# Optimization experiments

Hardware: AMD Instinct MI355X
Metric: run time of the kernel (lower is better)

## Reference

```python
import jax, jax.numpy as jnp
import numpy as np

DIM = 512
HEADS = 8
DHEAD = DIM // 8          # 64
INNER = HEADS * DHEAD     # 512
M_LANDMARKS = 256
PINV_ITERS = 6
KSZ = 33                  # residual depthwise conv kernel (default)


def setup_inputs() -> dict:
    key = jax.random.key(0)
    ks = jax.random.split(key, 5)
    B, N = 1, 16384
    s = DIM ** -0.5
    return {
        "x": jax.random.normal(ks[0], (B, N, DIM), jnp.float32),
        "norm_w": jnp.ones((DIM,), jnp.float32),
        "norm_b": jnp.zeros((DIM,), jnp.float32),
        "w_qkv": jax.random.normal(ks[1], (3 * INNER, DIM), jnp.float32) * s,   # Linear(dim, 3*inner, bias=False)
        "w_out": jax.random.normal(ks[2], (DIM, INNER), jnp.float32) * s,        # Linear(inner, dim)
        "b_out": jnp.zeros((DIM,), jnp.float32),
        "conv_w": jax.random.normal(ks[3], (HEADS, 1, KSZ, 1), jnp.float32) * 0.1,  # depthwise Conv2d(h,h,(33,1),groups=h)
    }


def _layernorm(x, w, b, eps=1e-5):
    mu = x.mean(-1, keepdims=True)
    var = ((x - mu) ** 2).mean(-1, keepdims=True)
    return (x - mu) * jax.lax.rsqrt(var + eps) * w + b


def _moore_penrose_pinv(a, iters):
    # a: [B, H, m, m]; matches lucidrains moore_penrose_iter_pinv (global max over col/row sums)
    abs_a = jnp.abs(a)
    col = abs_a.sum(-1).max()
    row = abs_a.sum(-2).max()
    z = jnp.swapaxes(a, -1, -2) / (col * row)
    I = jnp.eye(a.shape[-1], dtype=a.dtype)
    for _ in range(iters):
        az = a @ z
        z = 0.25 * z @ (13 * I - az @ (15 * I - az @ (7 * I - az)))
    return z


def _nystrom_attention(h, w_qkv, w_out, b_out, conv_w):
    B, N, _ = h.shape
    qkv = h @ w_qkv.T                          # [B, N, 3*inner]
    q, k, v = jnp.split(qkv, 3, axis=-1)

    def heads(t):
        return t.reshape(B, N, HEADS, DHEAD).transpose(0, 2, 1, 3)  # [B, H, N, d]
    q = heads(q) * (DHEAD ** -0.5)
    k = heads(k)
    v = heads(v)

    # landmark pooling: mean over contiguous groups of size l = N / m
    l = N // M_LANDMARKS
    q_l = q.reshape(B, HEADS, M_LANDMARKS, l, DHEAD).mean(3)   # [B, H, m, d]
    k_l = k.reshape(B, HEADS, M_LANDMARKS, l, DHEAD).mean(3)

    attn1 = jax.nn.softmax(jnp.einsum('bhnd,bhmd->bhnm', q, k_l), axis=-1)      # [B,H,N,m]
    attn2 = jax.nn.softmax(jnp.einsum('bhid,bhjd->bhij', q_l, k_l), axis=-1)    # [B,H,m,m]
    attn3 = jax.nn.softmax(jnp.einsum('bhmd,bhnd->bhmn', q_l, k), axis=-1)      # [B,H,m,N]

    attn2_inv = _moore_penrose_pinv(attn2, PINV_ITERS)
    out = attn1 @ (attn2_inv @ (attn3 @ v))                                     # [B,H,N,d]

    # residual depthwise conv along sequence dim (kernel 33x1, groups=HEADS, no bias)
    conv = jax.lax.conv_general_dilated(
        v, conv_w, window_strides=(1, 1),
        padding=((KSZ // 2, KSZ // 2), (0, 0)),
        dimension_numbers=('NCHW', 'OIHW', 'NCHW'),
        feature_group_count=HEADS)
    out = out + conv

    out = out.transpose(0, 2, 1, 3).reshape(B, N, INNER)
    return out @ w_out.T + b_out


def reference(x, norm_w, norm_b, w_qkv, w_out, b_out, conv_w):
    h = _layernorm(x, norm_w, norm_b)
    return x + _nystrom_attention(h, w_qkv, w_out, b_out, conv_w)
```

## Files before the change

### kernel.cpp

```cpp
#include <hip/hip_runtime.h>
#include <hip/hip_bf16.h>


typedef __attribute__((ext_vector_type(8))) short bf16x8;
typedef __attribute__((ext_vector_type(4))) float f32x4;

#define MFMA16(A, B, C) __builtin_amdgcn_mfma_f32_16x16x32_bf16(A, B, C, 0, 0, 0)
#define GLD16(g, l) __builtin_amdgcn_global_load_lds( \
    (const __attribute__((address_space(1))) void*)(g), \
    (__attribute__((address_space(3))) void*)(l), 16, 0, 0)

static __device__ __forceinline__ unsigned short f2b(float f) {
  __hip_bfloat16 h = __float2bfloat16(f);
  return *reinterpret_cast<unsigned short*>(&h);
}
static __device__ __forceinline__ float b2f(unsigned short u) {
  return __uint_as_float(((unsigned)u) << 16);
}

__global__ __launch_bounds__(256) void k_init(const float* __restrict__ x,
    const float* __restrict__ nw, const float* __restrict__ nb,
    unsigned short* __restrict__ h,
    const float* __restrict__ wq, unsigned short* __restrict__ wqb,
    const float* __restrict__ wo, unsigned short* __restrict__ wob) {
  const int b = blockIdx.x;
  const int t = threadIdx.x;
  if (b < 8192) {
    const int row = b * 2 + (t >> 7);
    const int tl = t & 127;
    const float4 xv = ((const float4*)(x + (size_t)row * 512))[tl];
    float s  = xv.x + xv.y + xv.z + xv.w;
    float sq = xv.x*xv.x + xv.y*xv.y + xv.z*xv.z + xv.w*xv.w;
    #pragma unroll
    for (int o = 32; o > 0; o >>= 1) {
      s  += __shfl_down(s, o, 64);
      sq += __shfl_down(sq, o, 64);
    }
    __shared__ float ls[4], lq[4];
    if ((t & 63) == 0) { ls[t >> 6] = s; lq[t >> 6] = sq; }
    __syncthreads();
    const int base = (t >> 7) << 1;
    s = ls[base] + ls[base + 1]; sq = lq[base] + lq[base + 1];
    const float mean = s * (1.0f / 512.0f);
    const float var  = sq * (1.0f / 512.0f) - mean * mean;
    const float rstd = rsqrtf(var + 1e-5f);
    const float4 wv = ((const float4*)nw)[tl];
    const float4 bv = ((const float4*)nb)[tl];
    ushort4 hv;
    hv.x = f2b((xv.x - mean) * rstd * wv.x + bv.x);
    hv.y = f2b((xv.y - mean) * rstd * wv.y + bv.y);
    hv.z = f2b((xv.z - mean) * rstd * wv.z + bv.z);
    hv.w = f2b((xv.w - mean) * rstd * wv.w + bv.w);
    ((ushort4*)(h + (size_t)row * 512))[tl] = hv;
  } else if (b < 8960) {
    const int i = (b - 8192) * 256 + t;
    const float4 f = ((const float4*)wq)[i];
    ushort4 u;
    u.x = f2b(f.x); u.y = f2b(f.y); u.z = f2b(f.z); u.w = f2b(f.w);
    ((ushort4*)wqb)[i] = u;
  } else {
    const int i = (b - 8960) * 256 + t;
    const float4 f = ((const float4*)wo)[i];
    ushort4 u;
    u.x = f2b(f.x); u.y = f2b(f.y); u.z = f2b(f.z); u.w = f2b(f.w);
    ((ushort4*)wob)[i] = u;
  }
}

__global__ __launch_bounds__(256) void k_qkv_mfma(const unsigned short* __restrict__ A,
    const unsigned short* __restrict__ B,
    unsigned short* __restrict__ qb, unsigned short* __restrict__ kb,
    unsigned short* __restrict__ vb) {
  __shared__ __align__(16) unsigned short SB[8192];
  unsigned short* As = SB;
  unsigned short* Bs = SB + 4096;
  const int t = threadIdx.x;
  const int lane = t & 63, w = t >> 6;
  const int quad = lane >> 4, l15 = lane & 15;
  const int wm = (w >> 1) * 64, wn = (w & 1) * 64;
  const int bid = blockIdx.x;
  const int xcd = bid & 7, i0 = bid >> 3;
  const int by = xcd * 16 + i0 / 12, bx = i0 % 12;
  const int m0 = by * 128, n0 = bx * 128;
  f32x4 acc[4][4];
  #pragma unroll
  for (int i = 0; i < 4; ++i)
    #pragma unroll
    for (int j = 0; j < 4; ++j) acc[i][j] = (f32x4){0.f, 0.f, 0.f, 0.f};
  for (int k0 = 0; k0 < 512; k0 += 32) {
    __syncthreads();
    #pragma unroll
    for (int c = 0; c < 2; ++c) {
      const int slot = c * 256 + t;
      const int row = slot >> 2, seg = slot & 3;
      GLD16(A + (size_t)(m0 + row) * 512 + k0 + seg * 8, As + slot * 8);
      GLD16(B + (size_t)(n0 + row) * 512 + k0 + seg * 8, Bs + slot * 8);
    }
    __syncthreads();
    bf16x8 a[4], b[4];
    #pragma unroll
    for (int i = 0; i < 4; ++i)
      a[i] = *(const bf16x8*)(As + (wm + i * 16 + l15) * 32 + quad * 8);
    #pragma unroll
    for (int j = 0; j < 4; ++j)
      b[j] = *(const bf16x8*)(Bs + (wn + j * 16 + l15) * 32 + quad * 8);
    #pragma unroll
    for (int i = 0; i < 4; ++i)
      #pragma unroll
      for (int j = 0; j < 4; ++j)
        acc[i][j] = MFMA16(a[i], b[j], acc[i][j]);
  }
  #pragma unroll
  for (int hf = 0; hf < 2; ++hf) {
    const int colbase = n0 + hf * 64;
    const int part = colbase >> 9;
    const int head = (colbase & 511) >> 6;
    unsigned short* dst = (part == 0) ? qb : (part == 1) ? kb : vb;
    const float scale = (part == 0) ? 0.125f : 1.0f;
    __syncthreads();
    if ((w & 1) == hf) {
      #pragma unroll
      for (int i = 0; i < 4; ++i)
        #pragma unroll
        for (int j = 0; j < 4; ++j)
          #pragma unroll
          for (int r = 0; r < 4; ++r) {
            const int row = wm + i * 16 + quad * 4 + r;
            const int col = j * 16 + l15;
            SB[row * 64 + col] = f2b(acc[i][j][r] * scale);
          }
    }
    __syncthreads();
    const int row = t >> 1, seg = (t & 1) * 32;
    unsigned short* dp = dst + ((size_t)head * 16384 + m0 + row) * 64 + seg;
    #pragma unroll
    for (int kk = 0; kk < 4; ++kk)
      *(ulonglong2*)(dp + kk * 8) = *(const ulonglong2*)&SB[row * 64 + seg + kk * 8];
  }
}

__global__ __launch_bounds__(256) void k_prep(const unsigned short* __restrict__ vb,
    unsigned short* __restrict__ vt, const unsigned short* __restrict__ qb,
    const unsigned short* __restrict__ kb, float* __restrict__ qlf,
    unsigned short* __restrict__ qlb, float* __restrict__ klf,
    unsigned short* __restrict__ klb) {
  __shared__ __align__(16) unsigned char smem[64 * 72 * 2];
  const int t = threadIdx.x;
  const int h = blockIdx.y;
  if (blockIdx.z == 0) {
    auto T = (unsigned short(*)[72])smem;
    const int n0 = blockIdx.x * 64;
    const int n = t >> 2, sg = (t & 3) * 16;
    const unsigned short* p = vb + ((size_t)(h * 16384 + n0 + n)) * 64 + sg;
    #pragma unroll
    for (int i = 0; i < 16; i += 4) {
      const ushort4 u = *(const ushort4*)(p + i);
      T[sg + i + 0][n] = u.x; T[sg + i + 1][n] = u.y;
      T[sg + i + 2][n] = u.z; T[sg + i + 3][n] = u.w;
    }
    __syncthreads();
    const int d = t >> 2, so = (t & 3) * 16;
    unsigned short* q = vt + ((size_t)(h * 64 + d)) * 16384 + n0 + so;
    #pragma unroll
    for (int i = 0; i < 16; i += 4) {
      ushort4 u;
      u.x = T[d][so + i]; u.y = T[d][so + i + 1];
      u.z = T[d][so + i + 2]; u.w = T[d][so + i + 3];
      *(ushort4*)(q + i) = u;
    }
  } else {
    auto red = (float(*)[64])smem;
    const int d = t & 63, grp = t >> 6;
    const int m = blockIdx.x;
    const unsigned short* src = (blockIdx.z == 1) ? qb : kb;
    const unsigned short* p = src + ((size_t)h * 16384 + m * 64 + grp * 16) * 64 + d;
    float s = 0.f;
    #pragma unroll
    for (int i = 0; i < 16; ++i) s += b2f(p[(size_t)i * 64]);
    red[grp][d] = s;
    __syncthreads();
    if (t < 64) {
      float v = (red[0][d] + red[1][d]) + (red[2][d] + red[3][d]);
      v *= (1.0f / 64.0f);
      const size_t oi = ((size_t)h * 256 + m) * 64 + d;
      if (blockIdx.z == 1) { qlf[oi] = v; qlb[oi] = f2b(v); }
      else                 { klf[oi] = v; klb[oi] = f2b(v); }
    }
  }
}

__global__ __launch_bounds__(256) void k_attn2(const float* __restrict__ ql,
    const float* __restrict__ kl, float* __restrict__ a2, unsigned short* __restrict__ a2b,
    float* __restrict__ csum) {
  const int i = blockIdx.x, h = blockIdx.y, j = threadIdx.x;
  __shared__ float qrow[64];
  __shared__ float wred[4];
  __shared__ float wsum[4];
  if (j < 64) qrow[j] = ql[((size_t)h * 256 + i) * 64 + j];
  __syncthreads();
  const float* kr = kl + ((size_t)h * 256 + j) * 64;
  float s = 0.f;
  #pragma unroll 8
  for (int d = 0; d < 64; ++d) s += qrow[d] * kr[d];
  float mx = s;
  #pragma unroll
  for (int o2 = 32; o2 > 0; o2 >>= 1) mx = fmaxf(mx, __shfl_xor(mx, o2, 64));
  if ((j & 63) == 0) wred[j >> 6] = mx;
  __syncthreads();
  mx = fmaxf(fmaxf(wred[0], wred[1]), fmaxf(wred[2], wred[3]));
  const float e = __expf(s - mx);
  float sm = e;
  #pragma unroll
  for (int o2 = 32; o2 > 0; o2 >>= 1) sm += __shfl_xor(sm, o2, 64);
  if ((j & 63) == 0) wsum[j >> 6] = sm;
  __syncthreads();
  sm = wsum[0] + wsum[1] + wsum[2] + wsum[3];
  const float v = e / sm;
  const size_t idx = ((size_t)h * 256 + i) * 256 + j;
  a2[idx] = v;
  a2b[idx] = f2b(v);
  atomicAdd(&csum[h * 256 + j], v);
}

__global__ __launch_bounds__(256) void k_z0(const float* __restrict__ a2,
    const float* __restrict__ csum, unsigned short* __restrict__ z0b,
    unsigned short* __restrict__ z0t) {
  __shared__ float T[64][65];
  __shared__ float wm[4];
  const int bi = blockIdx.x, bj = blockIdx.y, h = blockIdx.z;
  const int t = threadIdx.x;
  const int r = t >> 2, cseg = (t & 3) * 16;
  float m = 0.f;
  #pragma unroll
  for (int c = 0; c < 8; ++c) m = fmaxf(m, csum[c * 256 + t]);
  #pragma unroll
  for (int o2 = 32; o2 > 0; o2 >>= 1) m = fmaxf(m, __shfl_xor(m, o2, 64));
  if ((t & 63) == 0) wm[t >> 6] = m;
  __syncthreads();
  const float g = fmaxf(fmaxf(wm[0], wm[1]), fmaxf(wm[2], wm[3]));
  const float inv = 1.0f / g;
  const float* p = a2 + ((size_t)h * 256 + bj * 64 + r) * 256 + bi * 64 + cseg;
  unsigned short* qt = z0t + ((size_t)h * 256 + bj * 64 + r) * 256 + bi * 64 + cseg;
  #pragma unroll
  for (int i = 0; i < 16; i += 4) {
    const float4 f = *(const float4*)(p + i);
    T[cseg + i + 0][r] = f.x; T[cseg + i + 1][r] = f.y;
    T[cseg + i + 2][r] = f.z; T[cseg + i + 3][r] = f.w;
    ushort4 u;
    u.x = f2b(f.x * inv); u.y = f2b(f.y * inv);
    u.z = f2b(f.z * inv); u.w = f2b(f.w * inv);
    *(ushort4*)(qt + i) = u;
  }
  __syncthreads();
  unsigned short* qb_ = z0b + ((size_t)h * 256 + bi * 64 + r) * 256 + bj * 64 + cseg;
  #pragma unroll
  for (int i = 0; i < 16; i += 4) {
    ushort4 u;
    u.x = f2b(T[r][cseg + i] * inv);     u.y = f2b(T[r][cseg + i + 1] * inv);
    u.z = f2b(T[r][cseg + i + 2] * inv); u.w = f2b(T[r][cseg + i + 3] * inv);
    *(ushort4*)(qb_ + i) = u;
  }
}

__global__ __launch_bounds__(256) void k_pgemm(const unsigned short* __restrict__ A,
    const unsigned short* __restrict__ Bt, unsigned short* __restrict__ Cn,
    unsigned short* __restrict__ Ct, float* __restrict__ Cf,
    float alpha, float sdiag, int use_diag) {
  __shared__ unsigned short As[64 * 256];
  __shared__ unsigned short Bs[32 * 256];
  const int t = threadIdx.x;
  const int lane = t & 63, w = t >> 6;
  const int quad = lane >> 4, l15 = lane & 15;
  const int bn = blockIdx.x, bm = blockIdx.y, h = blockIdx.z;
  const size_t hs = (size_t)h * 65536;
  const unsigned short* Ap = A + hs + (size_t)(bm * 64) * 256;
  const unsigned short* Bp = Bt + hs + (size_t)(bn * 32) * 256;
  #pragma unroll
  for (int c = 0; c < 8; ++c) {
    const int s = c * 256 + t;
    const int row = s >> 5, pc = s & 31;
    const int lc = pc ^ (row & 7);
    GLD16(Ap + (size_t)row * 256 + lc * 8, As + s * 8);
  }
  #pragma unroll
  for (int c = 0; c < 4; ++c) {
    const int s = c * 256 + t;
    const int row = s >> 5, pc = s & 31;
    const int lc = pc ^ (row & 7);
    GLD16(Bp + (size_t)row * 256 + lc * 8, Bs + s * 8);
  }
  f32x4 acc[2];
  acc[0] = (f32x4){0.f, 0.f, 0.f, 0.f};
  acc[1] = (f32x4){0.f, 0.f, 0.f, 0.f};
  __syncthreads();
  const int arow = w * 16 + l15;
  #pragma unroll
  for (int kc = 0; kc < 8; ++kc) {
    const bf16x8 a = *(const bf16x8*)(As + arow * 256 + (((kc * 4 + quad) ^ (arow & 7)) * 8));
    #pragma unroll
    for (int j = 0; j < 2; ++j) {
      const int brow = j * 16 + l15;
      const bf16x8 b = *(const bf16x8*)(Bs + brow * 256 + (((kc * 4 + quad) ^ (brow & 7)) * 8));
      acc[j] = MFMA16(a, b, acc[j]);
    }
  }
  const int row0 = bm * 64 + w * 16 + quad * 4;
  #pragma unroll
  for (int j = 0; j < 2; ++j) {
    const int col = bn * 32 + j * 16 + l15;
    float v[4];
    #pragma unroll
    for (int r = 0; r < 4; ++r) v[r] = acc[j][r] * alpha;
    if (Cn) {
      #pragma unroll
      for (int r = 0; r < 4; ++r) Cn[hs + (size_t)(row0 + r) * 256 + col] = f2b(v[r]);
    }
    if (Cf) {
      #pragma unroll
      for (int r = 0; r < 4; ++r) Cf[hs + (size_t)(row0 + r) * 256 + col] = v[r];
    }
    ushort4 u;
    float tv[4];
    #pragma unroll
    for (int r = 0; r < 4; ++r)
      tv[r] = use_diag ? ((col == row0 + r ? sdiag : 0.f) - v[r]) : v[r];
    u.x = f2b(tv[0]); u.y = f2b(tv[1]); u.z = f2b(tv[2]); u.w = f2b(tv[3]);
    *(ushort4*)(Ct + hs + (size_t)col * 256 + row0) = u;
  }
}

__global__ __launch_bounds__(256) void k_gemm256(const float* __restrict__ A,
    const float* __restrict__ B, float* __restrict__ C,
    float alpha, float sdiag, int use_diag) {
  A += (size_t)blockIdx.z * 65536;
  B += (size_t)blockIdx.z * 65536;
  C += (size_t)blockIdx.z * 65536;
  __shared__ float As[16][68];
  __shared__ float Bs[16][36];
  const int t = threadIdx.x, tx = t & 15, ty = t >> 4;
  const int bn = blockIdx.x, bm = blockIdx.y;
  const int lr = t >> 2, lk = (t & 3) << 2;
  const int bkr = t >> 4, bnc = (t & 15) << 1;
  float acc[4][2] = {{0.f}};
  for (int k0 = 0; k0 < 256; k0 += 16) {
    float4 a4 = *(const float4*)(A + (size_t)(bm * 64 + lr) * 256 + k0 + lk);
    float2 b2 = *(const float2*)(B + (size_t)(k0 + bkr) * 256 + bn * 32 + bnc);
    if (use_diag) {
      const int kg = k0 + bkr, ngb = bn * 32 + bnc;
      b2.x = (kg == ngb + 0 ? sdiag : 0.f) - b2.x;
      b2.y = (kg == ngb + 1 ? sdiag : 0.f) - b2.y;
    }
    __syncthreads();
    As[lk+0][lr] = a4.x; As[lk+1][lr] = a4.y; As[lk+2][lr] = a4.z; As[lk+3][lr] = a4.w;
    Bs[bkr][bnc] = b2.x; Bs[bkr][bnc + 1] = b2.y;
    __syncthreads();
    #pragma unroll
    for (int kq = 0; kq < 16; ++kq) {
      const float4 av = *(const float4*)&As[kq][ty << 2];
      const float bx_ = Bs[kq][tx << 1], by_ = Bs[kq][(tx << 1) + 1];
      acc[0][0] += av.x * bx_; acc[0][1] += av.x * by_;
      acc[1][0] += av.y * bx_; acc[1][1] += av.y * by_;
      acc[2][0] += av.z * bx_; acc[2][1] += av.z * by_;
      acc[3][0] += av.w * bx_; acc[3][1] += av.w * by_;
    }
  }
  #pragma unroll
  for (int ii = 0; ii < 4; ++ii)
    #pragma unroll
    for (int jj = 0; jj < 2; ++jj)
      C[(size_t)(bm * 64 + (ty << 2) + ii) * 256 + bn * 32 + (tx << 1) + jj] =
          alpha * acc[ii][jj];
}

__global__ __launch_bounds__(256) void k_gemmD(const float* __restrict__ A,
    const float* __restrict__ B, const float* __restrict__ rs,
    unsigned short* __restrict__ dtb) {
  __shared__ float Asf[16 * 68];
  __shared__ float Bsf[16 * 68];
  const int bm = blockIdx.x, h = blockIdx.y;
  A += (size_t)h * 65536;
  B += (size_t)h * 16384;
  rs += (size_t)h * 256;
  const int t = threadIdx.x, tx = t & 15, ty = t >> 4;
  const int lr = t >> 2, lk = (t & 3) << 2;
  const int bkr = t >> 4, bnc = (t & 15) << 2;
  float acc[4][4] = {{0.f}};
  for (int k0 = 0; k0 < 256; k0 += 16) {
    float4 a4 = *(const float4*)(A + (size_t)(bm * 64 + lr) * 256 + k0 + lk);
    float4 b4 = *(const float4*)(B + (size_t)(k0 + bkr) * 64 + bnc);
    const float rv = 1.0f / rs[k0 + bkr];
    b4.x *= rv; b4.y *= rv; b4.z *= rv; b4.w *= rv;
    __syncthreads();
    Asf[(lk + 0) * 68 + lr] = a4.x; Asf[(lk + 1) * 68 + lr] = a4.y;
    Asf[(lk + 2) * 68 + lr] = a4.z; Asf[(lk + 3) * 68 + lr] = a4.w;
    *(float4*)&Bsf[bkr * 68 + bnc] = b4;
    __syncthreads();
    #pragma unroll
    for (int kq = 0; kq < 16; ++kq) {
      const float4 av = *(const float4*)&Asf[kq * 68 + (ty << 2)];
      const float4 bv = *(const float4*)&Bsf[kq * 68 + (tx << 2)];
      acc[0][0] += av.x*bv.x; acc[0][1] += av.x*bv.y; acc[0][2] += av.x*bv.z; acc[0][3] += av.x*bv.w;
      acc[1][0] += av.y*bv.x; acc[1][1] += av.y*bv.y; acc[1][2] += av.y*bv.z; acc[1][3] += av.y*bv.w;
      acc[2][0] += av.z*bv.x; acc[2][1] += av.z*bv.y; acc[2][2] += av.z*bv.z; acc[2][3] += av.z*bv.w;
      acc[3][0] += av.w*bv.x; acc[3][1] += av.w*bv.y; acc[3][2] += av.w*bv.z; acc[3][3] += av.w*bv.w;
    }
  }
  #pragma unroll
  for (int ii = 0; ii < 4; ++ii)
    #pragma unroll
    for (int jj = 0; jj < 4; ++jj)
      dtb[(size_t)(h * 64 + (tx << 2) + jj) * 256 + bm * 64 + (ty << 2) + ii] =
          f2b(acc[ii][jj]);
}

__global__ __launch_bounds__(256) void k_w3_mfma(const unsigned short* __restrict__ qlb,
    const unsigned short* __restrict__ kb, const unsigned short* __restrict__ vt,
    float* __restrict__ W, float* __restrict__ lsum) {
  __shared__ unsigned short QLs[64 * 64];
  __shared__ unsigned short Ks [64 * 64];
  __shared__ unsigned short Vts[64 * 64];
  __shared__ unsigned short Ps [64 * 64];
  const int t = threadIdx.x;
  const int lane = t & 63, w = t >> 6;
  const int quad = lane >> 4, l15 = lane & 15;
  const int kc = blockIdx.x, mt = blockIdx.y, h = blockIdx.z;
  #pragma unroll
  for (int c = 0; c < 2; ++c) {
    const int slot = c * 256 + t;
    const int row = slot >> 3, pc = slot & 7, lc = pc ^ (row & 7);
    GLD16(qlb + ((size_t)(h * 256 + mt * 64 + row)) * 64 + lc * 8, QLs + slot * 8);
  }
  __syncthreads();
  const int arow = w * 16 + l15;
  const bf16x8 aq0 = *(const bf16x8*)(QLs + arow * 64 + ((quad    ) ^ (arow & 7)) * 8);
  const bf16x8 aq1 = *(const bf16x8*)(QLs + arow * 64 + ((quad + 4) ^ (arow & 7)) * 8);
  f32x4 wacc[4];
  #pragma unroll
  for (int dt = 0; dt < 4; ++dt) wacc[dt] = (f32x4){0.f, 0.f, 0.f, 0.f};
  float lacc[4] = {0.f, 0.f, 0.f, 0.f};
  for (int ss = 0; ss < 16; ++ss) {
    const int n0 = kc * 1024 + ss * 64;
    __syncthreads();
    #pragma unroll
    for (int c = 0; c < 2; ++c) {
      const int slot = c * 256 + t;
      const int row = slot >> 3, pc = slot & 7, lc = pc ^ (row & 7);
      GLD16(kb + ((size_t)(h * 16384 + n0 + row)) * 64 + lc * 8, Ks + slot * 8);
      GLD16(vt + ((size_t)(h * 64 + row)) * 16384 + n0 + lc * 8, Vts + slot * 8);
    }
    __syncthreads();
    f32x4 s[4];
    #pragma unroll
    for (int j = 0; j < 4; ++j) {
      s[j] = (f32x4){0.f, 0.f, 0.f, 0.f};
      const int brow = j * 16 + l15;
      const bf16x8 b0 = *(const bf16x8*)(Ks + brow * 64 + ((quad    ) ^ (brow & 7)) * 8);
      const bf16x8 b1 = *(const bf16x8*)(Ks + brow * 64 + ((quad + 4) ^ (brow & 7)) * 8);
      s[j] = MFMA16(aq0, b0, s[j]);
      s[j] = MFMA16(aq1, b1, s[j]);
    }
    #pragma unroll
    for (int j = 0; j < 4; ++j)
      #pragma unroll
      for (int r = 0; r < 4; ++r) {
        const float e = __expf(s[j][r]);
        lacc[r] += e;
        const int prow = w * 16 + quad * 4 + r, pcol = j * 16 + l15;
        Ps[prow * 64 + (((pcol >> 3) ^ (prow & 7)) << 3) + (pcol & 7)] = f2b(e);
      }
    __syncthreads();
    const bf16x8 ap0 = *(const bf16x8*)(Ps + arow * 64 + ((quad    ) ^ (arow & 7)) * 8);
    const bf16x8 ap1 = *(const bf16x8*)(Ps + arow * 64 + ((quad + 4) ^ (arow & 7)) * 8);
    #pragma unroll
    for (int dt = 0; dt < 4; ++dt) {
      const int brow = dt * 16 + l15;
      const bf16x8 b0 = *(const bf16x8*)(Vts + brow * 64 + ((quad    ) ^ (brow & 7)) * 8);
      const bf16x8 b1 = *(const bf16x8*)(Vts + brow * 64 + ((quad + 4) ^ (brow & 7)) * 8);
      wacc[dt] = MFMA16(ap0, b0, wacc[dt]);
      wacc[dt] = MFMA16(ap1, b1, wacc[dt]);
    }
  }
  #pragma unroll
  for (int dt = 0; dt < 4; ++dt)
    #pragma unroll
    for (int r = 0; r < 4; ++r)
      atomicAdd(&W[((size_t)(h * 256 + mt * 64 + w * 16 + quad * 4 + r)) * 64 + dt * 16 + l15],
                wacc[dt][r]);
  #pragma unroll
  for (int r = 0; r < 4; ++r) {
    #pragma unroll
    for (int msk = 1; msk < 16; msk <<= 1) lacc[r] += __shfl_xor(lacc[r], msk, 64);
    if (l15 == 0)
      atomicAdd(&lsum[h * 256 + mt * 64 + w * 16 + quad * 4 + r], lacc[r]);
  }
}

__global__ __launch_bounds__(512) void k_attn1_mfma(const unsigned short* __restrict__ qb,
    const unsigned short* __restrict__ klb, const unsigned short* __restrict__ dtb,
    const unsigned short* __restrict__ vt, const float* __restrict__ cw,
    unsigned short* __restrict__ o) {
  __shared__ __align__(16) unsigned short Wb[2][6144];
  __shared__ unsigned short Ks[4096];
  __shared__ unsigned short Ds[4096];
  __shared__ unsigned short Ps[2][4096];
  __shared__ float Wsm[33];
  const int t = threadIdx.x;
  const int lane = t & 63, w = t >> 6;
  const int g = w >> 2, wl = w & 3;
  const int quad = lane >> 4, l15 = lane & 15;
  const int bt = blockIdx.x, h = blockIdx.y;
  const int n0 = bt * 128;
  if (t < 33) Wsm[t] = cw[h * 33 + t];
  unsigned short* WbF = &Wb[0][0];
  #pragma unroll
  for (int c = 0; c < 2; ++c) {
    const int slot = c * 512 + t;
    const int row = slot >> 3, pc = slot & 7, lc = pc ^ (row & 7);
    GLD16(qb + ((size_t)(h * 16384 + n0 + row)) * 64 + lc * 8, WbF + slot * 8);
  }
  __syncthreads();
  const int arow = wl * 16 + l15;
  const int qrow = g * 64 + arow;
  const bf16x8 aq0 = *(const bf16x8*)(WbF + qrow * 64 + ((quad    ) ^ (qrow & 7)) * 8);
  const bf16x8 aq1 = *(const bf16x8*)(WbF + qrow * 64 + ((quad + 4) ^ (qrow & 7)) * 8);
  __syncthreads();
  {
    const int gg = t >> 8;
    const int tl = t & 255;
    const int n = tl >> 2;
    const int gb = (tl & 3) * 24;
    #pragma unroll
    for (int i = 0; i < 24; ++i) {
      const int gc = gb + i;
      const int j = gc - n;
      const int src = n0 + gg * 64 - 16 + gc;
      const float val = (j >= 0 && j <= 32 && src >= 0 && src < 16384) ? Wsm[j] : 0.f;
      Wb[gg][n * 96 + (((gc >> 3) ^ (n & 3)) << 3) + (gc & 7)] = f2b(val);
    }
  }
  __syncthreads();
  f32x4 cacc[4];
  #pragma unroll
  for (int dt = 0; dt < 4; ++dt) cacc[dt] = (f32x4){0.f, 0.f, 0.f, 0.f};
  #pragma unroll
  for (int kcc = 0; kcc < 3; ++kcc) {
    const bf16x8 a = *(const bf16x8*)(&Wb[g][0] + arow * 96 + (((kcc * 4 + quad) ^ (arow & 3)) << 3));
    int off = n0 + g * 64 - 16 + kcc * 32 + quad * 8;
    off = off < 0 ? 0 : (off > 16376 ? 16376 : off);
    #pragma unroll
    for (int dt = 0; dt < 4; ++dt) {
      const bf16x8 b = *(const bf16x8*)(vt + ((size_t)(h * 64 + dt * 16 + l15)) * 16384 + off);
      cacc[dt] = MFMA16(a, b, cacc[dt]);
    }
  }
  f32x4 oacc[4];
  #pragma unroll
  for (int dt = 0; dt < 4; ++dt) oacc[dt] = (f32x4){0.f, 0.f, 0.f, 0.f};
  float lacc[4] = {0.f, 0.f, 0.f, 0.f};
  for (int mc = 0; mc < 4; ++mc) {
    const int m0 = mc * 64;
    __syncthreads();
    {
      const int row = t >> 3, pc = t & 7, lc = pc ^ (row & 7);
      GLD16(klb + ((size_t)(h * 256 + m0 + row)) * 64 + lc * 8, Ks + t * 8);
      GLD16(dtb + ((size_t)(h * 64 + row)) * 256 + m0 + lc * 8, Ds + t * 8);
    }
    __syncthreads();
    f32x4 s[4];
    #pragma unroll
    for (int j = 0; j < 4; ++j) {
      s[j] = (f32x4){0.f, 0.f, 0.f, 0.f};
      const int brow = j * 16 + l15;
      const bf16x8 b0 = *(const bf16x8*)(Ks + brow * 64 + ((quad    ) ^ (brow & 7)) * 8);
      const bf16x8 b1 = *(const bf16x8*)(Ks + brow * 64 + ((quad + 4) ^ (brow & 7)) * 8);
      s[j] = MFMA16(aq0, b0, s[j]);
      s[j] = MFMA16(aq1, b1, s[j]);
    }
    #pragma unroll
    for (int j = 0; j < 4; ++j)
      #pragma unroll
      for (int r = 0; r < 4; ++r) {
        const float e = __expf(s[j][r]);
        lacc[r] += e;
        const int prow = wl * 16 + quad * 4 + r, pcol = j * 16 + l15;
        Ps[g][prow * 64 + (((pcol >> 3) ^ (prow & 7)) << 3) + (pcol & 7)] = f2b(e);
      }
    __syncthreads();
    const bf16x8 ap0 = *(const bf16x8*)(&Ps[g][0] + arow * 64 + ((quad    ) ^ (arow & 7)) * 8);
    const bf16x8 ap1 = *(const bf16x8*)(&Ps[g][0] + arow * 64 + ((quad + 4) ^ (arow & 7)) * 8);
    #pragma unroll
    for (int dt = 0; dt < 4; ++dt) {
      const int brow = dt * 16 + l15;
      const bf16x8 b0 = *(const bf16x8*)(Ds + brow * 64 + ((quad    ) ^ (brow & 7)) * 8);
      const bf16x8 b1 = *(const bf16x8*)(Ds + brow * 64 + ((quad + 4) ^ (brow & 7)) * 8);
      oacc[dt] = MFMA16(ap0, b0, oacc[dt]);
      oacc[dt] = MFMA16(ap1, b1, oacc[dt]);
    }
  }
  #pragma unroll
  for (int r = 0; r < 4; ++r)
    #pragma unroll
    for (int msk = 1; msk < 16; msk <<= 1) lacc[r] += __shfl_xor(lacc[r], msk, 64);
  #pragma unroll
  for (int dt = 0; dt < 4; ++dt)
    #pragma unroll
    for (int r = 0; r < 4; ++r) {
      const float val = oacc[dt][r] / lacc[r] + cacc[dt][r];
      o[((size_t)(n0 + g * 64 + wl * 16 + quad * 4 + r)) * 512 + h * 64 + dt * 16 + l15] = f2b(val);
    }
}

__global__ __launch_bounds__(256) void k_out_mfma(const unsigned short* __restrict__ A,
    const unsigned short* __restrict__ B, const float* __restrict__ bias,
    const float* __restrict__ xres, float* __restrict__ out) {
  __shared__ unsigned short As[128 * 32];
  __shared__ unsigned short Bs[128 * 32];
  const int t = threadIdx.x;
  const int lane = t & 63, w = t >> 6;
  const int quad = lane >> 4, l15 = lane & 15;
  const int wm = (w >> 1) * 64, wn = (w & 1) * 64;
  const int bid = blockIdx.x;
  const int xcd = bid & 7, i0 = bid >> 3;
  const int by = xcd * 16 + (i0 >> 2), bx = i0 & 3;
  const int m0 = by * 128, n0 = bx * 128;
  f32x4 acc[4][4];
  #pragma unroll
  for (int i = 0; i < 4; ++i)
    #pragma unroll
    for (int j = 0; j < 4; ++j) acc[i][j] = (f32x4){0.f, 0.f, 0.f, 0.f};
  for (int k0 = 0; k0 < 512; k0 += 32) {
    __syncthreads();
    #pragma unroll
    for (int c = 0; c < 2; ++c) {
      const int slot = c * 256 + t;
      const int row = slot >> 2, seg = slot & 3;
      GLD16(A + (size_t)(m0 + row) * 512 + k0 + seg * 8, As + slot * 8);
      GLD16(B + (size_t)(n0 + row) * 512 + k0 + seg * 8, Bs + slot * 8);
    }
    __syncthreads();
    bf16x8 a[4], b[4];
    #pragma unroll
    for (int i = 0; i < 4; ++i)
      a[i] = *(const bf16x8*)(As + (wm + i * 16 + l15) * 32 + quad * 8);
    #pragma unroll
    for (int j = 0; j < 4; ++j)
      b[j] = *(const bf16x8*)(Bs + (wn + j * 16 + l15) * 32 + quad * 8);
    #pragma unroll
    for (int i = 0; i < 4; ++i)
      #pragma unroll
      for (int j = 0; j < 4; ++j)
        acc[i][j] = MFMA16(a[i], b[j], acc[i][j]);
  }
  #pragma unroll
  for (int i = 0; i < 4; ++i)
    #pragma unroll
    for (int j = 0; j < 4; ++j)
      #pragma unroll
      for (int r = 0; r < 4; ++r) {
        const int row = m0 + wm + i * 16 + quad * 4 + r;
        const int col = n0 + wn + j * 16 + l15;
        out[(size_t)row * 512 + col] = acc[i][j][r] + bias[col] + xres[(size_t)row * 512 + col];
      }
}

extern "C" void kernel_launch(void* const* d_in, const int* in_sizes, int n_in,
                              void* d_out, int out_size, void* d_ws, size_t ws_size,
                              hipStream_t stream) {
  const float* x      = (const float*)d_in[0];
  const float* norm_w = (const float*)d_in[1];
  const float* norm_b = (const float*)d_in[2];
  const float* w_qkv  = (const float*)d_in[3];
  const float* w_out  = (const float*)d_in[4];
  const float* b_out  = (const float*)d_in[5];
  const float* conv_w = (const float*)d_in[6];
  float* out = (float*)d_out;

  char* cur = (char*)d_ws;
  auto alloc = [&](size_t bytes) -> char* {
    char* p = cur;
    cur += (bytes + 255) & ~(size_t)255;
    return p;
  };
  const size_t NB = (size_t)16384 * 512;
  const size_t LM = (size_t)8 * 256 * 64;
  const size_t SQ = (size_t)8 * 256 * 256;

  unsigned short* h_b  = (unsigned short*)alloc(NB * 2);
  unsigned short* wq_b = (unsigned short*)alloc((size_t)1536 * 512 * 2);
  unsigned short* wo_b = (unsigned short*)alloc((size_t)512 * 512 * 2);
  unsigned short* qb   = (unsigned short*)alloc(NB * 2);
  unsigned short* kb   = (unsigned short*)alloc(NB * 2);
  unsigned short* vb   = (unsigned short*)alloc(NB * 2);
  unsigned short* vt   = (unsigned short*)alloc(NB * 2);
  float*          qlf  = (float*)alloc(LM * 4);
  float*          klf  = (float*)alloc(LM * 4);
  unsigned short* qlb  = (unsigned short*)alloc(LM * 2);
  unsigned short* klb  = (unsigned short*)alloc(LM * 2);
  float*          a2   = (float*)alloc(SQ * 4);
  unsigned short* a2b  = (unsigned short*)alloc(SQ * 2);
  unsigned short* z0b  = (unsigned short*)alloc(SQ * 2);
  unsigned short* z0t  = (unsigned short*)alloc(SQ * 2);
  unsigned short* Pn   = (unsigned short*)alloc(SQ * 2);
  unsigned short* Pt   = (unsigned short*)alloc(SQ * 2);
  unsigned short* Q1t  = (unsigned short*)alloc(SQ * 2);
  unsigned short* Q2t  = (unsigned short*)alloc(SQ * 2);
  unsigned short* zp0n = (unsigned short*)alloc(SQ * 2);
  unsigned short* zp0t = (unsigned short*)alloc(SQ * 2);
  unsigned short* zp1n = (unsigned short*)alloc(SQ * 2);
  unsigned short* zp1t = (unsigned short*)alloc(SQ * 2);
  float*          zf5  = (float*)alloc(SQ * 4);
  float*          zfin = (float*)alloc(SQ * 4);
  float*          Pp   = (float*)alloc(SQ * 4);
  float*          Q1   = (float*)alloc(SQ * 4);
  float*          Q2   = (float*)alloc(SQ * 4);
  float*          W    = (float*)alloc(LM * 4 + 4096 * 4);
  float*          lsum = W + LM;
  float*          csum = W + LM + 2048;
  unsigned short* dtb  = (unsigned short*)alloc(LM * 2);
  unsigned short* o_b  = (unsigned short*)alloc(NB * 2);

  hipMemsetAsync(W, 0, (LM + 4096) * sizeof(float), stream);
  k_init<<<9216, 256, 0, stream>>>(x, norm_w, norm_b, h_b, w_qkv, wq_b, w_out, wo_b);
  k_qkv_mfma<<<1536, 256, 0, stream>>>(h_b, wq_b, qb, kb, vb);
  k_prep<<<dim3(256, 8, 3), 256, 0, stream>>>(vb, vt, qb, kb, qlf, qlb, klf, klb);
  k_attn2<<<dim3(256, 8), 256, 0, stream>>>(qlf, klf, a2, a2b, csum);
  k_z0<<<dim3(4, 4, 8), 256, 0, stream>>>(a2, csum, z0b, z0t);
  k_w3_mfma<<<dim3(16, 4, 8), 256, 0, stream>>>(qlb, kb, vt, W, lsum);

  unsigned short* zan = z0b; unsigned short* zat = z0t;
  for (int it = 0; it < 5; ++it) {
    unsigned short* zbn = (it & 1) ? zp1n : zp0n;
    unsigned short* zbt = (it & 1) ? zp1t : zp0t;
    k_pgemm<<<dim3(8, 4, 8), 256, 0, stream>>>(a2b, zat, Pn, Pt, nullptr, 1.f, 7.f, 1);
    k_pgemm<<<dim3(8, 4, 8), 256, 0, stream>>>(Pn, Pt, nullptr, Q1t, nullptr, 1.f, 15.f, 1);
    k_pgemm<<<dim3(8, 4, 8), 256, 0, stream>>>(Pn, Q1t, nullptr, Q2t, nullptr, 1.f, 13.f, 1);
    k_pgemm<<<dim3(8, 4, 8), 256, 0, stream>>>(zan, Q2t, zbn, zbt,
        it == 4 ? zf5 : nullptr, 0.25f, 0.f, 0);
    zan = zbn; zat = zbt;
  }
  k_gemm256<<<dim3(8, 4, 8), 256, 0, stream>>>(a2, zf5, Pp, 1.f, 0.f, 0);
  k_gemm256<<<dim3(8, 4, 8), 256, 0, stream>>>(Pp, Pp, Q1, 1.f, 7.f, 1);
  k_gemm256<<<dim3(8, 4, 8), 256, 0, stream>>>(Pp, Q1, Q2, 1.f, 15.f, 1);
  k_gemm256<<<dim3(8, 4, 8), 256, 0, stream>>>(zf5, Q2, zfin, 0.25f, 13.f, 1);

  k_gemmD<<<dim3(4, 8), 256, 0, stream>>>(zfin, W, lsum, dtb);

  k_attn1_mfma<<<dim3(128, 8), 512, 0, stream>>>(qb, klb, dtb, vt, conv_w, o_b);
  k_out_mfma<<<512, 256, 0, stream>>>(o_b, wo_b, b_out, x, out);
}
```

Baseline: 418.4 us.

## Reuse K/V tiles across all landmark rows in w3; store QKV directly

The attn3·V kernel now has each block load all 256 landmark query rows and loop over four 64-row tiles. Each streamed K/V tile is reused four times instead of being reloaded by four separate blocks, and the grid shrinks from 512 to 128 blocks. The QKV GEMM epilogue drops its LDS-staged, vectorized 16-byte stores in favour of direct per-element bf16 stores into the head-major layout. This removes two barriers and the LDS round-trip but produces narrower, less coalesced global writes. The smaller w3 grid also leaves many CUs idle and raises per-thread accumulator register pressure.

```diff
diff --git a/kernel.cpp b/kernel.cpp
--- a/kernel.cpp
+++ b/kernel.cpp
@@ -71,9 +71,8 @@
     const unsigned short* __restrict__ B,
     unsigned short* __restrict__ qb, unsigned short* __restrict__ kb,
     unsigned short* __restrict__ vb) {
-  __shared__ __align__(16) unsigned short SB[8192];
-  unsigned short* As = SB;
-  unsigned short* Bs = SB + 4096;
+  __shared__ unsigned short As[128 * 32];
+  __shared__ unsigned short Bs[128 * 32];
   const int t = threadIdx.x;
   const int lane = t & 63, w = t >> 6;
   const int quad = lane >> 4, l15 = lane & 15;
@@ -110,33 +109,23 @@
       for (int j = 0; j < 4; ++j)
         acc[i][j] = MFMA16(a[i], b[j], acc[i][j]);
   }
-  #pragma unroll
-  for (int hf = 0; hf < 2; ++hf) {
-    const int colbase = n0 + hf * 64;
-    const int part = colbase >> 9;
-    const int head = (colbase & 511) >> 6;
-    unsigned short* dst = (part == 0) ? qb : (part == 1) ? kb : vb;
-    const float scale = (part == 0) ? 0.125f : 1.0f;
-    __syncthreads();
-    if ((w & 1) == hf) {
-      #pragma unroll
-      for (int i = 0; i < 4; ++i)
-        #pragma unroll
-        for (int j = 0; j < 4; ++j)
-          #pragma unroll
-          for (int r = 0; r < 4; ++r) {
-            const int row = wm + i * 16 + quad * 4 + r;
-            const int col = j * 16 + l15;
-            SB[row * 64 + col] = f2b(acc[i][j][r] * scale);
-          }
-    }
-    __syncthreads();
-    const int row = t >> 1, seg = (t & 1) * 32;
-    unsigned short* dp = dst + ((size_t)head * 16384 + m0 + row) * 64 + seg;
-    #pragma unroll
-    for (int kk = 0; kk < 4; ++kk)
-      *(ulonglong2*)(dp + kk * 8) = *(const ulonglong2*)&SB[row * 64 + seg + kk * 8];
-  }
+  const int part = n0 >> 9;
+  #pragma unroll
+  for (int i = 0; i < 4; ++i)
+    #pragma unroll
+    for (int j = 0; j < 4; ++j)
+      #pragma unroll
+      for (int r = 0; r < 4; ++r) {
+        const int row = m0 + wm + i * 16 + quad * 4 + r;
+        const int col = n0 + wn + j * 16 + l15;
+        const int rem = col & 511;
+        const int hd = rem >> 6, dd = rem & 63;
+        const size_t idx = ((size_t)hd * 16384 + row) * 64 + dd;
+        const float val = acc[i][j][r];
+        if (part == 0)      qb[idx] = f2b(val * 0.125f);
+        else if (part == 1) kb[idx] = f2b(val);
+        else                vb[idx] = f2b(val);
+      }
 }
 
 __global__ __launch_bounds__(256) void k_prep(const unsigned short* __restrict__ vb,
@@ -416,28 +405,32 @@
 __global__ __launch_bounds__(256) void k_w3_mfma(const unsigned short* __restrict__ qlb,
     const unsigned short* __restrict__ kb, const unsigned short* __restrict__ vt,
     float* __restrict__ W, float* __restrict__ lsum) {
-  __shared__ unsigned short QLs[64 * 64];
+  __shared__ unsigned short QLs[256 * 64];
   __shared__ unsigned short Ks [64 * 64];
   __shared__ unsigned short Vts[64 * 64];
   __shared__ unsigned short Ps [64 * 64];
   const int t = threadIdx.x;
   const int lane = t & 63, w = t >> 6;
   const int quad = lane >> 4, l15 = lane & 15;
-  const int kc = blockIdx.x, mt = blockIdx.y, h = blockIdx.z;
-  #pragma unroll
-  for (int c = 0; c < 2; ++c) {
+  const int kc = blockIdx.x, h = blockIdx.y;
+  #pragma unroll
+  for (int c = 0; c < 8; ++c) {
     const int slot = c * 256 + t;
     const int row = slot >> 3, pc = slot & 7, lc = pc ^ (row & 7);
-    GLD16(qlb + ((size_t)(h * 256 + mt * 64 + row)) * 64 + lc * 8, QLs + slot * 8);
+    GLD16(qlb + ((size_t)(h * 256 + row)) * 64 + lc * 8, QLs + slot * 8);
   }
   __syncthreads();
   const int arow = w * 16 + l15;
-  const bf16x8 aq0 = *(const bf16x8*)(QLs + arow * 64 + ((quad    ) ^ (arow & 7)) * 8);
-  const bf16x8 aq1 = *(const bf16x8*)(QLs + arow * 64 + ((quad + 4) ^ (arow & 7)) * 8);
-  f32x4 wacc[4];
-  #pragma unroll
-  for (int dt = 0; dt < 4; ++dt) wacc[dt] = (f32x4){0.f, 0.f, 0.f, 0.f};
-  float lacc[4] = {0.f, 0.f, 0.f, 0.f};
+  f32x4 wacc[4][4];
+  #pragma unroll
+  for (int mt = 0; mt < 4; ++mt)
+    #pragma unroll
+    for (int dt = 0; dt < 4; ++dt) wacc[mt][dt] = (f32x4){0.f, 0.f, 0.f, 0.f};
+  float lacc[4][4];
+  #pragma unroll
+  for (int mt = 0; mt < 4; ++mt)
+    #pragma unroll
+    for (int r = 0; r < 4; ++r) lacc[mt][r] = 0.f;
   for (int ss = 0; ss < 16; ++ss) {
     const int n0 = kc * 1024 + ss * 64;
     __syncthreads();
@@ -449,49 +442,58 @@
       GLD16(vt + ((size_t)(h * 64 + row)) * 16384 + n0 + lc * 8, Vts + slot * 8);
     }
     __syncthreads();
-    f32x4 s[4];
-    #pragma unroll
-    for (int j = 0; j < 4; ++j) {
-      s[j] = (f32x4){0.f, 0.f, 0.f, 0.f};
-      const int brow = j * 16 + l15;
-      const bf16x8 b0 = *(const bf16x8*)(Ks + brow * 64 + ((quad    ) ^ (brow & 7)) * 8);
-      const bf16x8 b1 = *(const bf16x8*)(Ks + brow * 64 + ((quad + 4) ^ (brow & 7)) * 8);
-      s[j] = MFMA16(aq0, b0, s[j]);
-      s[j] = MFMA16(aq1, b1, s[j]);
-    }
-    #pragma unroll
-    for (int j = 0; j < 4; ++j)
-      #pragma unroll
-      for (int r = 0; r < 4; ++r) {
-        const float e = __expf(s[j][r]);
-        lacc[r] += e;
-        const int prow = w * 16 + quad * 4 + r, pcol = j * 16 + l15;
-        Ps[prow * 64 + (((pcol >> 3) ^ (prow & 7)) << 3) + (pcol & 7)] = f2b(e);
+    #pragma unroll 1
+    for (int mt = 0; mt < 4; ++mt) {
+      const int qrow = mt * 64 + arow;
+      const bf16x8 aq0 = *(const bf16x8*)(QLs + qrow * 64 + ((quad    ) ^ (qrow & 7)) * 8);
+      const bf16x8 aq1 = *(const bf16x8*)(QLs + qrow * 64 + ((quad + 4) ^ (qrow & 7)) * 8);
+      f32x4 s[4];
+      #pragma unroll
+      for (int j = 0; j < 4; ++j) {
+        s[j] = (f32x4){0.f, 0.f, 0.f, 0.f};
+        const int brow = j * 16 + l15;
+        const bf16x8 b0 = *(const bf16x8*)(Ks + brow * 64 + ((quad    ) ^ (brow & 7)) * 8);
+        const bf16x8 b1 = *(const bf16x8*)(Ks + brow * 64 + ((quad + 4) ^ (brow & 7)) * 8);
+        s[j] = MFMA16(aq0, b0, s[j]);
+        s[j] = MFMA16(aq1, b1, s[j]);
       }
-    __syncthreads();
-    const bf16x8 ap0 = *(const bf16x8*)(Ps + arow * 64 + ((quad    ) ^ (arow & 7)) * 8);
-    const bf16x8 ap1 = *(const bf16x8*)(Ps + arow * 64 + ((quad + 4) ^ (arow & 7)) * 8);
-    #pragma unroll
-    for (int dt = 0; dt < 4; ++dt) {
-      const int brow = dt * 16 + l15;
-      const bf16x8 b0 = *(const bf16x8*)(Vts + brow * 64 + ((quad    ) ^ (brow & 7)) * 8);
-      const bf16x8 b1 = *(const bf16x8*)(Vts + brow * 64 + ((quad + 4) ^ (brow & 7)) * 8);
-      wacc[dt] = MFMA16(ap0, b0, wacc[dt]);
-      wacc[dt] = MFMA16(ap1, b1, wacc[dt]);
-    }
-  }
-  #pragma unroll
-  for (int dt = 0; dt < 4; ++dt)
-    #pragma unroll
-    for (int r = 0; r < 4; ++r)
-      atomicAdd(&W[((size_t)(h * 256 + mt * 64 + w * 16 + quad * 4 + r)) * 64 + dt * 16 + l15],
-                wacc[dt][r]);
-  #pragma unroll
-  for (int r = 0; r < 4; ++r) {
-    #pragma unroll
-    for (int msk = 1; msk < 16; msk <<= 1) lacc[r] += __shfl_xor(lacc[r], msk, 64);
-    if (l15 == 0)
-      atomicAdd(&lsum[h * 256 + mt * 64 + w * 16 + quad * 4 + r], lacc[r]);
+      #pragma unroll
+      for (int j = 0; j < 4; ++j)
+        #pragma unroll
+        for (int r = 0; r < 4; ++r) {
+          const float e = __expf(s[j][r]);
+          lacc[mt][r] += e;
+          const int prow = w * 16 + quad * 4 + r, pcol = j * 16 + l15;
+          Ps[prow * 64 + (((pcol >> 3) ^ (prow & 7)) << 3) + (pcol & 7)] = f2b(e);
+        }
+      const bf16x8 ap0 = *(const bf16x8*)(Ps + arow * 64 + ((quad    ) ^ (arow & 7)) * 8);
+      const bf16x8 ap1 = *(const bf16x8*)(Ps + arow * 64 + ((quad + 4) ^ (arow & 7)) * 8);
+      #pragma unroll
+      for (int dt = 0; dt < 4; ++dt) {
+        const int brow = dt * 16 + l15;
+        const bf16x8 b0 = *(const bf16x8*)(Vts + brow * 64 + ((quad    ) ^ (brow & 7)) * 8);
+        const bf16x8 b1 = *(const bf16x8*)(Vts + brow * 64 + ((quad + 4) ^ (brow & 7)) * 8);
+        wacc[mt][dt] = MFMA16(ap0, b0, wacc[mt][dt]);
+        wacc[mt][dt] = MFMA16(ap1, b1, wacc[mt][dt]);
+      }
+    }
+  }
+  #pragma unroll
+  for (int mt = 0; mt < 4; ++mt) {
+    #pragma unroll
+    for (int dt = 0; dt < 4; ++dt)
+      #pragma unroll
+      for (int r = 0; r < 4; ++r)
+        atomicAdd(&W[((size_t)(h * 256 + mt * 64 + w * 16 + quad * 4 + r)) * 64 + dt * 16 + l15],
+                  wacc[mt][dt][r]);
+    #pragma unroll
+    for (int r = 0; r < 4; ++r) {
+      float lv = lacc[mt][r];
+      #pragma unroll
+      for (int msk = 1; msk < 16; msk <<= 1) lv += __shfl_xor(lv, msk, 64);
+      if (l15 == 0)
+        atomicAdd(&lsum[h * 256 + mt * 64 + w * 16 + quad * 4 + r], lv);
+    }
   }
 }
 
@@ -725,7 +727,7 @@
   k_prep<<<dim3(256, 8, 3), 256, 0, stream>>>(vb, vt, qb, kb, qlf, qlb, klf, klb);
   k_attn2<<<dim3(256, 8), 256, 0, stream>>>(qlf, klf, a2, a2b, csum);
   k_z0<<<dim3(4, 4, 8), 256, 0, stream>>>(a2, csum, z0b, z0t);
-  k_w3_mfma<<<dim3(16, 4, 8), 256, 0, stream>>>(qlb, kb, vt, W, lsum);
+  k_w3_mfma<<<dim3(16, 8), 256, 0, stream>>>(qlb, kb, vt, W, lsum);
 
   unsigned short* zan = z0b; unsigned short* zat = z0t;
   for (int it = 0; it < 5; ++it) {
```

Measured after the change: 472.3 us. 1.13x slower.
